# Kernel optimization log

Measured on AMD Instinct MI355X. Metric: run time of the kernel, lower is better.

The kernel has to match this reference:

```python
import jax, jax.numpy as jnp
import numpy as np

NEG = -1e9
EPS = 1e-3  # LayerNormalization eps in this repo


def sinusoid_table(n_position, d):
    pe = np.array([[p / np.power(10000, 2 * (j // 2) / d) for j in range(d)]
                   if p != 0 else np.zeros(d) for p in range(n_position)])
    pe[1:, 0::2] = np.sin(pe[1:, 0::2])
    pe[1:, 1::2] = np.cos(pe[1:, 1::2])
    return jnp.asarray(pe, jnp.float32)


def setup_inputs() -> dict:
    B, S, D, H, DK, DV, DFF, L, V = 16, 512, 512, 8, 64, 64, 1024, 6, 32000
    key = jax.random.key(0)
    ks = jax.random.split(key, 16)
    sc = 0.02
    word_emb = jax.random.normal(ks[0], (V, D), jnp.float32) * sc
    word_emb = word_emb.at[0].set(0.0)  # padding_idx=0
    pos_emb = sinusoid_table(S + 1, D)
    inp = {
        'src_seq': jax.random.randint(ks[1], (B, S), 1, V, jnp.int32),
        'src_pos': jnp.tile(jnp.arange(1, S + 1, dtype=jnp.int32)[None, :], (B, 1)),
        'word_emb': word_emb,
        'pos_emb': pos_emb,
        'Wq': jax.random.normal(ks[2], (L, H, D, DK), jnp.float32) * sc,
        'Wk': jax.random.normal(ks[3], (L, H, D, DK), jnp.float32) * sc,
        'Wv': jax.random.normal(ks[4], (L, H, D, DV), jnp.float32) * sc,
        'Wo': jax.random.normal(ks[5], (L, H * DV, D), jnp.float32) * sc,
        'bo': jnp.zeros((L, D), jnp.float32),
        'ln1_a': jnp.ones((L, D), jnp.float32),
        'ln1_b': jnp.zeros((L, D), jnp.float32),
        'w1': jax.random.normal(ks[6], (L, D, DFF), jnp.float32) * sc,
        'b1': jnp.zeros((L, DFF), jnp.float32),
        'w2': jax.random.normal(ks[7], (L, DFF, D), jnp.float32) * sc,
        'b2': jnp.zeros((L, D), jnp.float32),
        'ln2_a': jnp.ones((L, D), jnp.float32),
        'ln2_b': jnp.zeros((L, D), jnp.float32),
        'skip_w': jax.random.normal(ks[8], (L, D), jnp.float32) * sc,
        'skip_b': jnp.zeros((L,), jnp.float32),
    }
    return inp


def _layer_norm(z, a, b):
    mu = jnp.mean(z, axis=-1, keepdims=True)
    sd = jnp.std(z, axis=-1, keepdims=True, ddof=1)  # torch.std is unbiased
    return a * (z - mu) / (sd + EPS) + b


def _forward(src_seq, src_pos, word_emb, pos_emb, Wq, Wk, Wv, Wo, bo,
             ln1_a, ln1_b, w1, b1, w2, b2, ln2_a, ln2_b, skip_w, skip_b):
    B, S = src_seq.shape
    d_model = word_emb.shape[1]
    L, H = Wq.shape[0], Wq.shape[1]
    x = word_emb[src_seq] + pos_emb[src_pos]  # [B,S,D]
    rng = jax.random.key(42)
    scale = jnp.sqrt(jnp.float32(d_model))  # old-repo ScaledDotProductAttention temper
    for l in range(L):
        # --- SkippingProbability + ProbabilisticSkipper ---
        probs = jax.nn.sigmoid(jnp.einsum('bsd,d->bs', x, skip_w[l]) + skip_b[l])
        rng, sub = jax.random.split(rng)
        drop = jax.random.bernoulli(sub, jax.lax.stop_gradient(probs))  # noise ~ Bern(p)
        keep = ~drop  # keeping_timesteps = 1 - noise
        # stable compaction: kept timesteps to front, dropped positions zeroed (pad)
        order = jnp.argsort(jnp.where(keep, 0, 1), axis=1, stable=True)  # [B,S]
        x = jnp.take_along_axis(x, order[:, :, None], axis=1)
        x = x * jnp.take_along_axis(keep, order, axis=1)[:, :, None].astype(x.dtype)
        # pad mask recomputed from enc_input channel 0 (as in get_attn_padding_mask)
        pad = x[:, :, 0] == 0  # [B,S] True at padded keys
        # --- MultiHeadAttention ---
        residual = x
        q = jnp.einsum('bsd,hdk->bhsk', x, Wq[l])
        k = jnp.einsum('bsd,hdk->bhsk', x, Wk[l])
        v = jnp.einsum('bsd,hdv->bhsv', x, Wv[l])
        scores = jnp.einsum('bhqk,bhsk->bhqs', q, k) / scale
        scores = jnp.where(pad[:, None, None, :], NEG, scores)
        attn = jax.nn.softmax(scores, axis=-1)
        o = jnp.einsum('bhqs,bhsv->bhqv', attn, v)
        o = o.transpose(0, 2, 1, 3).reshape(B, S, -1)  # concat heads
        x = _layer_norm(o @ Wo[l] + bo[l] + residual, ln1_a[l], ln1_b[l])
        # --- PositionwiseFeedForwardFunnel ---
        h = jax.nn.relu(x @ w1[l] + b1[l]) @ w2[l] + b2[l]
        x = _layer_norm(h + x, ln2_a[l], ln2_b[l])
    return x


def reference(src_seq, src_pos, word_emb, pos_emb, Wq, Wk, Wv, Wo, bo,
              ln1_a, ln1_b, w1, b1, w2, b2, ln2_a, ln2_b, skip_w, skip_b):
    return _forward(src_seq, src_pos, word_emb, pos_emb, Wq, Wk, Wv, Wo, bo,
                    ln1_a, ln1_b, w1, b1, w2, b2, ln2_a, ln2_b, skip_w, skip_b)
```

## Files before the change

### kernel.cpp

```cpp
#include <hip/hip_runtime.h>
#include <math.h>

#define NEGV (-1e9f)
#define ISCALE 0.04419417382415922f

typedef __attribute__((ext_vector_type(8))) __bf16 bf16x8;
typedef __attribute__((ext_vector_type(4))) float f32x4;

__device__ inline unsigned short f2bf(float x){
  unsigned u = __float_as_uint(x);
  unsigned r = (u + 0x7fffu + ((u>>16)&1u)) >> 16;
  return (unsigned short)r;
}
__device__ inline float bf2f(unsigned short b){ return __uint_as_float((unsigned)b<<16); }

__host__ __device__ inline unsigned rotl32(unsigned v, int d){ return (v<<d)|(v>>(32-d)); }

__host__ __device__ inline void tf2x32(unsigned k0, unsigned k1, unsigned c0, unsigned c1,
                                       unsigned* o0, unsigned* o1){
  unsigned ks2 = k0 ^ k1 ^ 0x1BD11BDAu;
  unsigned x0 = c0 + k0, x1 = c1 + k1;
#define RND(r) { x0 += x1; x1 = rotl32(x1,(r)); x1 ^= x0; }
  RND(13) RND(15) RND(26) RND(6)   x0 += k1;  x1 += ks2 + 1u;
  RND(17) RND(29) RND(16) RND(24)  x0 += ks2; x1 += k0  + 2u;
  RND(13) RND(15) RND(26) RND(6)   x0 += k0;  x1 += k1  + 3u;
  RND(17) RND(29) RND(16) RND(24)  x0 += k1;  x1 += ks2 + 4u;
  RND(13) RND(15) RND(26) RND(6)   x0 += ks2; x1 += k0  + 5u;
#undef RND
  *o0 = x0; *o1 = x1;
}

__global__ void emb_kernel(const int* __restrict__ seq, const int* __restrict__ pos,
                           const float* __restrict__ we, const float* __restrict__ pe,
                           float* __restrict__ x){
  int t = blockIdx.x; int tid = threadIdx.x;
  int id = seq[t]; int pp = pos[t];
  float4 w = ((const float4*)(we + (size_t)id*512))[tid];
  float4 p = ((const float4*)(pe + (size_t)pp*512))[tid];
  float4 o; o.x=w.x+p.x; o.y=w.y+p.y; o.z=w.z+p.z; o.w=w.w+p.w;
  ((float4*)(x + (size_t)t*512))[tid] = o;
}

__global__ __launch_bounds__(64) void probs_keep_kernel(const float* __restrict__ x,
        const float* __restrict__ sw, const float* __restrict__ sb,
        unsigned k0, unsigned k1, int* __restrict__ keep){
  int t = blockIdx.x; int lane = threadIdx.x;
  const float* row = x + (size_t)t*512;
  float acc = 0.f;
  #pragma unroll
  for (int i=0;i<8;i++){ int d = lane + (i<<6); acc += row[d]*sw[d]; }
  #pragma unroll
  for (int o=32;o;o>>=1) acc += __shfl_xor(acc, o);
  if (lane==0){
    float z = acc + sb[0];
    float p = 1.f/(1.f + expf(-z));
    unsigned y0,y1; tf2x32(k0,k1, 0u,(unsigned)t, &y0,&y1);
    unsigned bits = y0 ^ y1;
    float u = __uint_as_float((bits>>9) | 0x3f800000u) - 1.0f;
    keep[t] = (u < p) ? 0 : 1;
  }
}

__global__ void scan_kernel(const int* __restrict__ keep, int* __restrict__ map,
                            int* __restrict__ nkeep){
  int b = blockIdx.x; int s = threadIdx.x;
  __shared__ int sc[512];
  int k = keep[(b<<9) + s];
  sc[s] = k;
  __syncthreads();
  for (int o=1;o<512;o<<=1){
    int t = (s>=o) ? sc[s-o] : 0;
    __syncthreads();
    sc[s] += t;
    __syncthreads();
  }
  if (k) map[(b<<9) + sc[s] - 1] = s;
  if (s==511) nkeep[b] = sc[511];
}

__global__ void gather_kernel(const float* __restrict__ src, float* __restrict__ dst,
                              const int* __restrict__ map, const int* __restrict__ nkeep){
  int blk = blockIdx.x; int b = blk >> 9; int j = blk & 511; int tid = threadIdx.x;
  float4* drow = (float4*)(dst + (size_t)blk*512);
  if (j < nkeep[b]){
    const float4* srow = (const float4*)(src + (size_t)((b<<9) + map[blk])*512);
    drow[tid] = srow[tid];
  } else {
    drow[tid] = make_float4(0.f,0.f,0.f,0.f);
  }
}

__global__ void wqkv_kernel(const float* __restrict__ Wq, const float* __restrict__ Wk,
                            const float* __restrict__ Wv, float* __restrict__ Wt){
  int d = blockIdx.x; int which = blockIdx.y; int c = threadIdx.x;
  const float* src = (which==0)? Wq : (which==1)? Wk : Wv;
  Wt[(size_t)d*1536 + (which<<9) + c] =
      src[(size_t)(c>>6)*32768 + ((size_t)d<<6) + (c&63)];
}

__global__ __launch_bounds__(256) void split3_kernel(const float* __restrict__ in,
        unsigned short* __restrict__ h, unsigned short* __restrict__ m,
        unsigned short* __restrict__ l, int n){
  int i = (blockIdx.x*256 + threadIdx.x) << 2;
  if (i >= n) return;
  float4 v = *(const float4*)(in + i);
  float xs[4] = {v.x, v.y, v.z, v.w};
  unsigned short ha[4], ma[4], la[4];
  #pragma unroll
  for (int j=0;j<4;j++){
    float x = xs[j];
    unsigned short hh = f2bf(x);
    float r1 = x - bf2f(hh);
    unsigned short mm = f2bf(r1);
    float r2 = r1 - bf2f(mm);
    ha[j]=hh; ma[j]=mm; la[j]=f2bf(r2);
  }
  *(ushort4*)(h+i) = make_ushort4(ha[0],ha[1],ha[2],ha[3]);
  *(ushort4*)(m+i) = make_ushort4(ma[0],ma[1],ma[2],ma[3]);
  *(ushort4*)(l+i) = make_ushort4(la[0],la[1],la[2],la[3]);
}

__global__ __launch_bounds__(256) void wsplit_kernel(const float* __restrict__ W,
        unsigned short* __restrict__ h, unsigned short* __restrict__ m,
        unsigned short* __restrict__ l, int K, int N){
  __shared__ float T[64][68];
  int k0 = blockIdx.y<<6, n0 = blockIdx.x<<6;
  int tid = threadIdx.x;
  int r = tid >> 4, c4 = tid & 15;
  #pragma unroll
  for (int rep=0; rep<4; rep++){
    int kk = r + (rep<<4);
    float4 v = *(const float4*)(W + (size_t)(k0+kk)*N + n0 + (c4<<2));
    *(float4*)&T[kk][c4<<2] = v;
  }
  __syncthreads();
  #pragma unroll
  for (int rep=0; rep<4; rep++){
    int nn = r + (rep<<4);
    int kk = c4<<2;
    unsigned short ha[4], ma[4], la[4];
    #pragma unroll
    for (int j=0;j<4;j++){
      float x = T[kk+j][nn];
      unsigned short hh = f2bf(x);
      float r1 = x - bf2f(hh);
      unsigned short mm = f2bf(r1);
      float r2 = r1 - bf2f(mm);
      ha[j]=hh; ma[j]=mm; la[j]=f2bf(r2);
    }
    size_t o = (size_t)(n0+nn)*K + k0 + kk;
    *(ushort4*)(h+o) = make_ushort4(ha[0],ha[1],ha[2],ha[3]);
    *(ushort4*)(m+o) = make_ushort4(ma[0],ma[1],ma[2],ma[3]);
    *(ushort4*)(l+o) = make_ushort4(la[0],la[1],la[2],la[3]);
  }
}

template<bool BIAS, bool RES, bool RELU>
__global__ __launch_bounds__(256) void gemm_mfma(
        const unsigned short* __restrict__ Ah, const unsigned short* __restrict__ Am2,
        const unsigned short* __restrict__ Al,
        const unsigned short* __restrict__ Bh, const unsigned short* __restrict__ Bm2,
        const unsigned short* __restrict__ Bl,
        const float* __restrict__ bias, const float* __restrict__ R,
        float* __restrict__ C, int M, int N, int K){
  __shared__ unsigned short As[3][128][40];
  __shared__ unsigned short Bs[3][128][40];
  int bn = blockIdx.x, bm = blockIdx.y;
  int tid = threadIdx.x;
  int w = tid >> 6, lane = tid & 63;
  int wm = w >> 1, wn = w & 1;
  int lrow = lane & 15, kg = lane >> 4;
  const unsigned short* Apl[3] = {Ah, Am2, Al};
  const unsigned short* Bpl[3] = {Bh, Bm2, Bl};

  f32x4 acc[4][4];
  const f32x4 zz = {0.f,0.f,0.f,0.f};
  #pragma unroll
  for (int i=0;i<4;i++)
    #pragma unroll
    for (int j=0;j<4;j++) acc[i][j] = zz;

  int srow = tid >> 1, seg = tid & 1;
  for (int ks = 0; ks < K; ks += 32){
    size_t abase = (size_t)(bm*128 + srow)*K + ks + seg*16;
    size_t bbase = (size_t)(bn*128 + srow)*K + ks + seg*16;
    #pragma unroll
    for (int p=0;p<3;p++){
      const unsigned short* ap = Apl[p] + abase;
      *(uint4*)&As[p][srow][seg*16]   = *(const uint4*)ap;
      *(uint4*)&As[p][srow][seg*16+8] = *(const uint4*)(ap+8);
      const unsigned short* bp = Bpl[p] + bbase;
      *(uint4*)&Bs[p][srow][seg*16]   = *(const uint4*)bp;
      *(uint4*)&Bs[p][srow][seg*16+8] = *(const uint4*)(bp+8);
    }
    __syncthreads();
    bf16x8 bfr[4][3];
    #pragma unroll
    for (int nf=0;nf<4;nf++)
      #pragma unroll
      for (int p=0;p<3;p++)
        bfr[nf][p] = *(const bf16x8*)&Bs[p][(wn<<6)+(nf<<4)+lrow][kg<<3];
    #pragma unroll
    for (int mf=0;mf<4;mf++){
      bf16x8 ah = *(const bf16x8*)&As[0][(wm<<6)+(mf<<4)+lrow][kg<<3];
      bf16x8 am = *(const bf16x8*)&As[1][(wm<<6)+(mf<<4)+lrow][kg<<3];
      bf16x8 al = *(const bf16x8*)&As[2][(wm<<6)+(mf<<4)+lrow][kg<<3];
      #pragma unroll
      for (int nf=0;nf<4;nf++){
        acc[mf][nf] = __builtin_amdgcn_mfma_f32_16x16x32_bf16(ah, bfr[nf][0], acc[mf][nf], 0,0,0);
        acc[mf][nf] = __builtin_amdgcn_mfma_f32_16x16x32_bf16(ah, bfr[nf][1], acc[mf][nf], 0,0,0);
        acc[mf][nf] = __builtin_amdgcn_mfma_f32_16x16x32_bf16(am, bfr[nf][0], acc[mf][nf], 0,0,0);
        acc[mf][nf] = __builtin_amdgcn_mfma_f32_16x16x32_bf16(ah, bfr[nf][2], acc[mf][nf], 0,0,0);
        acc[mf][nf] = __builtin_amdgcn_mfma_f32_16x16x32_bf16(al, bfr[nf][0], acc[mf][nf], 0,0,0);
        acc[mf][nf] = __builtin_amdgcn_mfma_f32_16x16x32_bf16(am, bfr[nf][1], acc[mf][nf], 0,0,0);
      }
    }
    __syncthreads();
  }
  int c0 = (bn<<7) + (wn<<6);
  int r0g = (bm<<7) + (wm<<6);
  #pragma unroll
  for (int mf=0;mf<4;mf++){
    #pragma unroll
    for (int nf=0;nf<4;nf++){
      int col = c0 + (nf<<4) + lrow;
      int rowb = r0g + (mf<<4) + (kg<<2);
      #pragma unroll
      for (int r=0;r<4;r++){
        float v = acc[mf][nf][r];
        if (BIAS) v += bias[col];
        if (RES)  v += R[(size_t)(rowb+r)*N + col];
        if (RELU) v = fmaxf(v, 0.f);
        C[(size_t)(rowb+r)*N + col] = v;
      }
    }
  }
}

template<bool BIAS, bool RES, bool RELU>
__global__ __launch_bounds__(256) void gemm_kernel(const float* __restrict__ A,
        const float* __restrict__ Bm, const float* __restrict__ bias,
        const float* __restrict__ R, float* __restrict__ C, int M, int N, int K){
  __shared__ float As[16][64];
  __shared__ float Bs[16][64];
  int bn = blockIdx.x, bm = blockIdx.y;
  int tid = threadIdx.x;
  int tx = tid & 15, ty = tid >> 4;
  int arow = tid >> 2,  acg = (tid & 3) << 2;
  int brow = tid >> 4,  bcg = (tid & 15) << 2;
  const float* Ab = A + (size_t)bm*64*K;
  const float* Bb = Bm + (bn<<6);
  float acc[4][4] = {};
  for (int k0 = 0; k0 < K; k0 += 16){
    float4 av = *(const float4*)(Ab + (size_t)arow*K + k0 + acg);
    float4 bv = *(const float4*)(Bb + (size_t)(k0+brow)*N + bcg);
    __syncthreads();
    As[acg+0][arow]=av.x; As[acg+1][arow]=av.y; As[acg+2][arow]=av.z; As[acg+3][arow]=av.w;
    *(float4*)&Bs[brow][bcg] = bv;
    __syncthreads();
    #pragma unroll
    for (int kk=0;kk<16;kk++){
      float4 a = *(const float4*)&As[kk][ty<<2];
      float4 b = *(const float4*)&Bs[kk][tx<<2];
      acc[0][0] += a.x*b.x; acc[0][1] += a.x*b.y; acc[0][2] += a.x*b.z; acc[0][3] += a.x*b.w;
      acc[1][0] += a.y*b.x; acc[1][1] += a.y*b.y; acc[1][2] += a.y*b.z; acc[1][3] += a.y*b.w;
      acc[2][0] += a.z*b.x; acc[2][1] += a.z*b.y; acc[2][2] += a.z*b.z; acc[2][3] += a.z*b.w;
      acc[3][0] += a.w*b.x; acc[3][1] += a.w*b.y; acc[3][2] += a.w*b.z; acc[3][3] += a.w*b.w;
    }
  }
  int row0 = (bm<<6) + (ty<<2), col0 = (bn<<6) + (tx<<2);
  #pragma unroll
  for (int i=0;i<4;i++){
    #pragma unroll
    for (int j=0;j<4;j++){
      float v = acc[i][j];
      if (BIAS) v += bias[col0+j];
      if (RES)  v += R[(size_t)(row0+i)*N + col0+j];
      if (RELU) v = fmaxf(v, 0.f);
      C[(size_t)(row0+i)*N + col0+j] = v;
    }
  }
}

__global__ __launch_bounds__(256) void fattn_kernel(const float* __restrict__ QKV,
        const float* __restrict__ Xc, float* __restrict__ O){
  __shared__ float QsT[64][68];
  __shared__ float KsT[64][68];
  __shared__ float Vs[64][68];
  __shared__ float PsT[64][68];
  __shared__ float pads[512];
  int orig = blockIdx.x;
  int wgid = ((orig & 7) << 7) + (orig >> 3);
  int qt = wgid & 7; int bh = wgid >> 3; int h = bh & 7; int b = bh >> 3;
  int tid = threadIdx.x;
  int d4 = tid & 15;
  int r0 = tid >> 4;
  size_t rowbase = (size_t)(b << 9) * 1536;
  int q0 = qt << 6;
  const float* Qg = QKV + rowbase + (size_t)q0*1536 + (h<<6);
  #pragma unroll
  for (int rep = 0; rep < 4; rep++){
    int q = r0 + (rep<<4);
    float4 v = *(const float4*)(Qg + (size_t)q*1536 + (d4<<2));
    QsT[(d4<<2)+0][q] = v.x; QsT[(d4<<2)+1][q] = v.y;
    QsT[(d4<<2)+2][q] = v.z; QsT[(d4<<2)+3][q] = v.w;
  }
  pads[tid]     = Xc[(size_t)((b<<9) + tid) << 9];
  pads[tid+256] = Xc[(size_t)((b<<9) + tid + 256) << 9];

  int tx = tid & 15, ty = tid >> 4;
  float m[4], l[4], out[4][4];
  #pragma unroll
  for (int i=0;i<4;i++){ m[i] = -3.0e38f; l[i] = 0.f;
    out[i][0]=0.f; out[i][1]=0.f; out[i][2]=0.f; out[i][3]=0.f; }
  const float* Kg = QKV + rowbase + 512 + (h<<6);
  const float* Vg = QKV + rowbase + 1024 + (h<<6);

  for (int kt = 0; kt < 8; kt++){
    __syncthreads();
    #pragma unroll
    for (int rep = 0; rep < 4; rep++){
      int k = r0 + (rep<<4);
      size_t krow = (size_t)((kt<<6) + k)*1536;
      float4 kv = *(const float4*)(Kg + krow + (d4<<2));
      KsT[(d4<<2)+0][k] = kv.x; KsT[(d4<<2)+1][k] = kv.y;
      KsT[(d4<<2)+2][k] = kv.z; KsT[(d4<<2)+3][k] = kv.w;
      float4 vv = *(const float4*)(Vg + krow + (d4<<2));
      *(float4*)&Vs[k][d4<<2] = vv;
    }
    __syncthreads();
    float acc[4][4] = {};
    #pragma unroll 4
    for (int d = 0; d < 64; d++){
      float4 a  = *(const float4*)&QsT[d][ty<<2];
      float4 bq = *(const float4*)&KsT[d][tx<<2];
      acc[0][0] += a.x*bq.x; acc[0][1] += a.x*bq.y; acc[0][2] += a.x*bq.z; acc[0][3] += a.x*bq.w;
      acc[1][0] += a.y*bq.x; acc[1][1] += a.y*bq.y; acc[1][2] += a.y*bq.z; acc[1][3] += a.y*bq.w;
      acc[2][0] += a.z*bq.x; acc[2][1] += a.z*bq.y; acc[2][2] += a.z*bq.z; acc[2][3] += a.z*bq.w;
      acc[3][0] += a.w*bq.x; acc[3][1] += a.w*bq.y; acc[3][2] += a.w*bq.z; acc[3][3] += a.w*bq.w;
    }
    int kbase = kt<<6;
    float sv[4][4];
    #pragma unroll
    for (int j=0;j<4;j++){
      bool pad = (pads[kbase + (tx<<2) + j] == 0.f);
      #pragma unroll
      for (int i=0;i<4;i++) sv[i][j] = pad ? NEGV : acc[i][j]*ISCALE;
    }
    #pragma unroll
    for (int i=0;i<4;i++){
      float tm = fmaxf(fmaxf(sv[i][0],sv[i][1]), fmaxf(sv[i][2],sv[i][3]));
      tm = fmaxf(tm, __shfl_xor(tm,1)); tm = fmaxf(tm, __shfl_xor(tm,2));
      tm = fmaxf(tm, __shfl_xor(tm,4)); tm = fmaxf(tm, __shfl_xor(tm,8));
      float mn = fmaxf(m[i], tm);
      float f  = expf(m[i] - mn);
      m[i] = mn;
      float rs = 0.f;
      #pragma unroll
      for (int j=0;j<4;j++){
        float e = expf(sv[i][j] - mn);
        sv[i][j] = e; rs += e;
      }
      rs += __shfl_xor(rs,1); rs += __shfl_xor(rs,2);
      rs += __shfl_xor(rs,4); rs += __shfl_xor(rs,8);
      l[i] = l[i]*f + rs;
      out[i][0]*=f; out[i][1]*=f; out[i][2]*=f; out[i][3]*=f;
    }
    #pragma unroll
    for (int j=0;j<4;j++){
      float4 pv = make_float4(sv[0][j], sv[1][j], sv[2][j], sv[3][j]);
      *(float4*)&PsT[(tx<<2)+j][ty<<2] = pv;
    }
    __syncthreads();
    #pragma unroll 4
    for (int k=0;k<64;k++){
      float4 a  = *(const float4*)&PsT[k][ty<<2];
      float4 bv = *(const float4*)&Vs[k][tx<<2];
      out[0][0] += a.x*bv.x; out[0][1] += a.x*bv.y; out[0][2] += a.x*bv.z; out[0][3] += a.x*bv.w;
      out[1][0] += a.y*bv.x; out[1][1] += a.y*bv.y; out[1][2] += a.y*bv.z; out[1][3] += a.y*bv.w;
      out[2][0] += a.z*bv.x; out[2][1] += a.z*bv.y; out[2][2] += a.z*bv.z; out[2][3] += a.z*bv.w;
      out[3][0] += a.w*bv.x; out[3][1] += a.w*bv.y; out[3][2] += a.w*bv.z; out[3][3] += a.w*bv.w;
    }
  }
  size_t obase = ((size_t)(b<<9) + q0) << 9;
  #pragma unroll
  for (int i=0;i<4;i++){
    float inv = 1.f / l[i];
    float4 ov = make_float4(out[i][0]*inv, out[i][1]*inv, out[i][2]*inv, out[i][3]*inv);
    *(float4*)(O + obase + (size_t)((ty<<2)+i)*512 + (h<<6) + (tx<<2)) = ov;
  }
}

__global__ __launch_bounds__(256) void ln_kernel(const float* __restrict__ in,
        const float* __restrict__ ga, const float* __restrict__ be, float* __restrict__ out){
  int t = blockIdx.x; int tid = threadIdx.x;
  const float* row = in + (size_t)t*512;
  float v0 = row[tid], v1 = row[tid+256];
  float s = v0 + v1;
  #pragma unroll
  for (int o=32;o;o>>=1) s += __shfl_xor(s,o);
  __shared__ float red[4];
  int wid = tid >> 6, lane = tid & 63;
  if (lane==0) red[wid] = s;
  __syncthreads();
  float mu = (red[0]+red[1]+red[2]+red[3]) * (1.f/512.f);
  float d0 = v0-mu, d1 = v1-mu;
  float q = d0*d0 + d1*d1;
  #pragma unroll
  for (int o=32;o;o>>=1) q += __shfl_xor(q,o);
  __syncthreads();
  if (lane==0) red[wid] = q;
  __syncthreads();
  float var = (red[0]+red[1]+red[2]+red[3]) * (1.f/511.f);
  float inv = 1.f/(sqrtf(var) + 1e-3f);
  float* orow = out + (size_t)t*512;
  orow[tid]     = ga[tid]    *(d0*inv) + be[tid];
  orow[tid+256] = ga[tid+256]*(d1*inv) + be[tid+256];
}

extern "C" void kernel_launch(void* const* d_in, const int* in_sizes, int n_in,
                              void* d_out, int out_size, void* d_ws, size_t ws_size,
                              hipStream_t stream){
  const int*   seq = (const int*)d_in[0];
  const int*   pos = (const int*)d_in[1];
  const float* we  = (const float*)d_in[2];
  const float* pe  = (const float*)d_in[3];
  const float* Wq  = (const float*)d_in[4];
  const float* Wk  = (const float*)d_in[5];
  const float* Wv  = (const float*)d_in[6];
  const float* Wo  = (const float*)d_in[7];
  const float* bo  = (const float*)d_in[8];
  const float* l1a = (const float*)d_in[9];
  const float* l1b = (const float*)d_in[10];
  const float* w1  = (const float*)d_in[11];
  const float* b1  = (const float*)d_in[12];
  const float* w2  = (const float*)d_in[13];
  const float* b2  = (const float*)d_in[14];
  const float* l2a = (const float*)d_in[15];
  const float* l2b = (const float*)d_in[16];
  const float* sw  = (const float*)d_in[17];
  const float* sb  = (const float*)d_in[18];
  float* out = (float*)d_out;

  const size_t TD = (size_t)8192*512;
  float* A    = (float*)d_ws;
  float* Bc   = A  + TD;
  float* QKVb = Bc + TD;
  float* P1   = QKVb;
  float* Hb   = QKVb + TD;
  float* Wt   = QKVb + 3*TD;
  int* keep = (int*)(Wt + (size_t)512*1536);
  int* map  = keep + 8192;
  int* nk   = map  + 8192;
  unsigned short* ap0 = (unsigned short*)(nk + 8192);
  const size_t APS = (size_t)8192*1024;
  unsigned short* ap1 = ap0 + APS;
  unsigned short* ap2 = ap1 + APS;
  unsigned short* wp0 = ap2 + APS;
  const size_t WPS = (size_t)1536*512;
  unsigned short* wp1 = wp0 + WPS;
  unsigned short* wp2 = wp1 + WPS;
  size_t need = (size_t)((char*)(wp2 + WPS) - (char*)d_ws);
  bool mfma_ok = (ws_size >= need);

  unsigned r0=0u, r1=42u, subs0[6], subs1[6];
  for (int l=0;l<6;l++){
    unsigned a0,a1,b0,b1;
    tf2x32(r0,r1, 0u,0u, &a0,&a1);
    tf2x32(r0,r1, 0u,1u, &b0,&b1);
    subs0[l]=b0; subs1[l]=b1; r0=a0; r1=a1;
  }

  emb_kernel<<<8192,128,0,stream>>>(seq,pos,we,pe,A);

  for (int l=0;l<6;l++){
    probs_keep_kernel<<<8192,64,0,stream>>>(A, sw + (size_t)l*512, sb + l,
                                            subs0[l], subs1[l], keep);
    scan_kernel<<<16,512,0,stream>>>(keep, map, nk);
    gather_kernel<<<8192,128,0,stream>>>(A, Bc, map, nk);
    wqkv_kernel<<<dim3(512,3),512,0,stream>>>(Wq + (size_t)l*262144,
                                              Wk + (size_t)l*262144,
                                              Wv + (size_t)l*262144, Wt);
    if (mfma_ok){
      split3_kernel<<<4096,256,0,stream>>>(Bc, ap0, ap1, ap2, 8192*512);
      wsplit_kernel<<<dim3(24,8),256,0,stream>>>(Wt, wp0, wp1, wp2, 512, 1536);
      gemm_mfma<false,false,false><<<dim3(12,64),256,0,stream>>>(ap0,ap1,ap2,
              wp0,wp1,wp2, nullptr, nullptr, QKVb, 8192,1536,512);
      fattn_kernel<<<1024,256,0,stream>>>(QKVb, Bc, A);
      split3_kernel<<<4096,256,0,stream>>>(A, ap0, ap1, ap2, 8192*512);
      wsplit_kernel<<<dim3(8,8),256,0,stream>>>(Wo + (size_t)l*262144, wp0, wp1, wp2, 512, 512);
      gemm_mfma<true,true,false><<<dim3(4,64),256,0,stream>>>(ap0,ap1,ap2,
              wp0,wp1,wp2, bo + (size_t)l*512, Bc, P1, 8192,512,512);
      ln_kernel<<<8192,256,0,stream>>>(P1, l1a + (size_t)l*512, l1b + (size_t)l*512, A);
      split3_kernel<<<4096,256,0,stream>>>(A, ap0, ap1, ap2, 8192*512);
      wsplit_kernel<<<dim3(16,8),256,0,stream>>>(w1 + (size_t)l*524288, wp0, wp1, wp2, 512, 1024);
      gemm_mfma<true,false,true><<<dim3(8,64),256,0,stream>>>(ap0,ap1,ap2,
              wp0,wp1,wp2, b1 + (size_t)l*1024, nullptr, Hb, 8192,1024,512);
      split3_kernel<<<8192,256,0,stream>>>(Hb, ap0, ap1, ap2, 8192*1024);
      wsplit_kernel<<<dim3(8,16),256,0,stream>>>(w2 + (size_t)l*524288, wp0, wp1, wp2, 1024, 512);
      gemm_mfma<true,true,false><<<dim3(4,64),256,0,stream>>>(ap0,ap1,ap2,
              wp0,wp1,wp2, b2 + (size_t)l*512, A, P1, 8192,512,1024);
    } else {
      gemm_kernel<false,false,false><<<dim3(24,128),256,0,stream>>>(Bc, Wt,
              nullptr, nullptr, QKVb, 8192,1536,512);
      fattn_kernel<<<1024,256,0,stream>>>(QKVb, Bc, A);
      gemm_kernel<true,true,false><<<dim3(8,128),256,0,stream>>>(A, Wo + (size_t)l*262144,
              bo + (size_t)l*512, Bc, P1, 8192,512,512);
      ln_kernel<<<8192,256,0,stream>>>(P1, l1a + (size_t)l*512, l1b + (size_t)l*512, A);
      gemm_kernel<true,false,true><<<dim3(16,128),256,0,stream>>>(A, w1 + (size_t)l*524288,
              b1 + (size_t)l*1024, nullptr, Hb, 8192,1024,512);
      gemm_kernel<true,true,false><<<dim3(8,128),256,0,stream>>>(Hb, w2 + (size_t)l*524288,
              b2 + (size_t)l*512, A, P1, 8192,512,1024);
    }
    ln_kernel<<<8192,256,0,stream>>>(P1, l2a + (size_t)l*512, l2b + (size_t)l*512,
                                     (l==5)? out : A);
  }
}
```

Measured before the change: 3.142 ms.

## Replace 3-way bf16 split GEMM with 2-way scaled fp16 split

Operands are now split into an fp16 high part and an fp16 residual scaled by 4096, replacing the three-part bf16 decomposition. Each GEMM issues three fp16 MFMAs per tile instead of six bf16 MFMAs and loads two planes instead of three. This cuts the split-kernel traffic, the LDS footprint and the tensor-core work. The trade-off is reduced accuracy and fp16 range limits: values beyond fp16 range, or residuals that underflow, could hurt fp32 emulation fidelity.

```diff
diff --git a/kernel.cpp b/kernel.cpp
--- a/kernel.cpp
+++ b/kernel.cpp
@@ -4,15 +4,16 @@
 #define NEGV (-1e9f)
 #define ISCALE 0.04419417382415922f
 
-typedef __attribute__((ext_vector_type(8))) __bf16 bf16x8;
+typedef __attribute__((ext_vector_type(8))) _Float16 f16x8;
+typedef __attribute__((ext_vector_type(4))) _Float16 f16x4;
 typedef __attribute__((ext_vector_type(4))) float f32x4;
 
-__device__ inline unsigned short f2bf(float x){
-  unsigned u = __float_as_uint(x);
-  unsigned r = (u + 0x7fffu + ((u>>16)&1u)) >> 16;
-  return (unsigned short)r;
-}
-__device__ inline float bf2f(unsigned short b){ return __uint_as_float((unsigned)b<<16); }
+__device__ inline void split2h(float x, _Float16& H, _Float16& M){
+  _Float16 h = (_Float16)x;
+  float m = x - (float)h;
+  H = h;
+  M = (_Float16)(m * 4096.0f);
+}
 
 __host__ __device__ inline unsigned rotl32(unsigned v, int d){ return (v<<d)|(v>>(32-d)); }
 
@@ -98,31 +99,21 @@
       src[(size_t)(c>>6)*32768 + ((size_t)d<<6) + (c&63)];
 }
 
-__global__ __launch_bounds__(256) void split3_kernel(const float* __restrict__ in,
-        unsigned short* __restrict__ h, unsigned short* __restrict__ m,
-        unsigned short* __restrict__ l, int n){
+__global__ __launch_bounds__(256) void split2_kernel(const float* __restrict__ in,
+        _Float16* __restrict__ h, _Float16* __restrict__ m, int n){
   int i = (blockIdx.x*256 + threadIdx.x) << 2;
   if (i >= n) return;
   float4 v = *(const float4*)(in + i);
   float xs[4] = {v.x, v.y, v.z, v.w};
-  unsigned short ha[4], ma[4], la[4];
-  #pragma unroll
-  for (int j=0;j<4;j++){
-    float x = xs[j];
-    unsigned short hh = f2bf(x);
-    float r1 = x - bf2f(hh);
-    unsigned short mm = f2bf(r1);
-    float r2 = r1 - bf2f(mm);
-    ha[j]=hh; ma[j]=mm; la[j]=f2bf(r2);
-  }
-  *(ushort4*)(h+i) = make_ushort4(ha[0],ha[1],ha[2],ha[3]);
-  *(ushort4*)(m+i) = make_ushort4(ma[0],ma[1],ma[2],ma[3]);
-  *(ushort4*)(l+i) = make_ushort4(la[0],la[1],la[2],la[3]);
+  f16x4 ha, ma;
+  #pragma unroll
+  for (int j=0;j<4;j++){ _Float16 H,M; split2h(xs[j],H,M); ha[j]=H; ma[j]=M; }
+  *(f16x4*)(h+i) = ha;
+  *(f16x4*)(m+i) = ma;
 }
 
 __global__ __launch_bounds__(256) void wsplit_kernel(const float* __restrict__ W,
-        unsigned short* __restrict__ h, unsigned short* __restrict__ m,
-        unsigned short* __restrict__ l, int K, int N){
+        _Float16* __restrict__ h, _Float16* __restrict__ m, int K, int N){
   __shared__ float T[64][68];
   int k0 = blockIdx.y<<6, n0 = blockIdx.x<<6;
   int tid = threadIdx.x;
@@ -138,81 +129,67 @@
   for (int rep=0; rep<4; rep++){
     int nn = r + (rep<<4);
     int kk = c4<<2;
-    unsigned short ha[4], ma[4], la[4];
-    #pragma unroll
-    for (int j=0;j<4;j++){
-      float x = T[kk+j][nn];
-      unsigned short hh = f2bf(x);
-      float r1 = x - bf2f(hh);
-      unsigned short mm = f2bf(r1);
-      float r2 = r1 - bf2f(mm);
-      ha[j]=hh; ma[j]=mm; la[j]=f2bf(r2);
-    }
+    f16x4 ha, ma;
+    #pragma unroll
+    for (int j=0;j<4;j++){ _Float16 H,M; split2h(T[kk+j][nn],H,M); ha[j]=H; ma[j]=M; }
     size_t o = (size_t)(n0+nn)*K + k0 + kk;
-    *(ushort4*)(h+o) = make_ushort4(ha[0],ha[1],ha[2],ha[3]);
-    *(ushort4*)(m+o) = make_ushort4(ma[0],ma[1],ma[2],ma[3]);
-    *(ushort4*)(l+o) = make_ushort4(la[0],la[1],la[2],la[3]);
+    *(f16x4*)(h+o) = ha;
+    *(f16x4*)(m+o) = ma;
   }
 }
 
 template<bool BIAS, bool RES, bool RELU>
 __global__ __launch_bounds__(256) void gemm_mfma(
-        const unsigned short* __restrict__ Ah, const unsigned short* __restrict__ Am2,
-        const unsigned short* __restrict__ Al,
-        const unsigned short* __restrict__ Bh, const unsigned short* __restrict__ Bm2,
-        const unsigned short* __restrict__ Bl,
+        const _Float16* __restrict__ Ah, const _Float16* __restrict__ Am,
+        const _Float16* __restrict__ Bh, const _Float16* __restrict__ Bm,
         const float* __restrict__ bias, const float* __restrict__ R,
         float* __restrict__ C, int M, int N, int K){
-  __shared__ unsigned short As[3][128][40];
-  __shared__ unsigned short Bs[3][128][40];
+  __shared__ _Float16 As[2][128][40];
+  __shared__ _Float16 Bs[2][128][40];
   int bn = blockIdx.x, bm = blockIdx.y;
   int tid = threadIdx.x;
   int w = tid >> 6, lane = tid & 63;
   int wm = w >> 1, wn = w & 1;
   int lrow = lane & 15, kg = lane >> 4;
-  const unsigned short* Apl[3] = {Ah, Am2, Al};
-  const unsigned short* Bpl[3] = {Bh, Bm2, Bl};
-
-  f32x4 acc[4][4];
+  const _Float16* Apl[2] = {Ah, Am};
+  const _Float16* Bpl[2] = {Bh, Bm};
+
+  f32x4 acc0[4][4], acc1[4][4];
   const f32x4 zz = {0.f,0.f,0.f,0.f};
   #pragma unroll
   for (int i=0;i<4;i++)
     #pragma unroll
-    for (int j=0;j<4;j++) acc[i][j] = zz;
+    for (int j=0;j<4;j++){ acc0[i][j] = zz; acc1[i][j] = zz; }
 
   int srow = tid >> 1, seg = tid & 1;
   for (int ks = 0; ks < K; ks += 32){
     size_t abase = (size_t)(bm*128 + srow)*K + ks + seg*16;
     size_t bbase = (size_t)(bn*128 + srow)*K + ks + seg*16;
     #pragma unroll
-    for (int p=0;p<3;p++){
-      const unsigned short* ap = Apl[p] + abase;
+    for (int p=0;p<2;p++){
+      const _Float16* ap = Apl[p] + abase;
       *(uint4*)&As[p][srow][seg*16]   = *(const uint4*)ap;
       *(uint4*)&As[p][srow][seg*16+8] = *(const uint4*)(ap+8);
-      const unsigned short* bp = Bpl[p] + bbase;
+      const _Float16* bp = Bpl[p] + bbase;
       *(uint4*)&Bs[p][srow][seg*16]   = *(const uint4*)bp;
       *(uint4*)&Bs[p][srow][seg*16+8] = *(const uint4*)(bp+8);
     }
     __syncthreads();
-    bf16x8 bfr[4][3];
+    f16x8 bfr[4][2];
     #pragma unroll
     for (int nf=0;nf<4;nf++)
       #pragma unroll
-      for (int p=0;p<3;p++)
-        bfr[nf][p] = *(const bf16x8*)&Bs[p][(wn<<6)+(nf<<4)+lrow][kg<<3];
+      for (int p=0;p<2;p++)
+        bfr[nf][p] = *(const f16x8*)&Bs[p][(wn<<6)+(nf<<4)+lrow][kg<<3];
     #pragma unroll
     for (int mf=0;mf<4;mf++){
-      bf16x8 ah = *(const bf16x8*)&As[0][(wm<<6)+(mf<<4)+lrow][kg<<3];
-      bf16x8 am = *(const bf16x8*)&As[1][(wm<<6)+(mf<<4)+lrow][kg<<3];
-      bf16x8 al = *(const bf16x8*)&As[2][(wm<<6)+(mf<<4)+lrow][kg<<3];
+      f16x8 ah = *(const f16x8*)&As[0][(wm<<6)+(mf<<4)+lrow][kg<<3];
+      f16x8 am = *(const f16x8*)&As[1][(wm<<6)+(mf<<4)+lrow][kg<<3];
       #pragma unroll
       for (int nf=0;nf<4;nf++){
-        acc[mf][nf] = __builtin_amdgcn_mfma_f32_16x16x32_bf16(ah, bfr[nf][0], acc[mf][nf], 0,0,0);
-        acc[mf][nf] = __builtin_amdgcn_mfma_f32_16x16x32_bf16(ah, bfr[nf][1], acc[mf][nf], 0,0,0);
-        acc[mf][nf] = __builtin_amdgcn_mfma_f32_16x16x32_bf16(am, bfr[nf][0], acc[mf][nf], 0,0,0);
-        acc[mf][nf] = __builtin_amdgcn_mfma_f32_16x16x32_bf16(ah, bfr[nf][2], acc[mf][nf], 0,0,0);
-        acc[mf][nf] = __builtin_amdgcn_mfma_f32_16x16x32_bf16(al, bfr[nf][0], acc[mf][nf], 0,0,0);
-        acc[mf][nf] = __builtin_amdgcn_mfma_f32_16x16x32_bf16(am, bfr[nf][1], acc[mf][nf], 0,0,0);
+        acc0[mf][nf] = __builtin_amdgcn_mfma_f32_16x16x32_f16(ah, bfr[nf][0], acc0[mf][nf], 0,0,0);
+        acc1[mf][nf] = __builtin_amdgcn_mfma_f32_16x16x32_f16(ah, bfr[nf][1], acc1[mf][nf], 0,0,0);
+        acc1[mf][nf] = __builtin_amdgcn_mfma_f32_16x16x32_f16(am, bfr[nf][0], acc1[mf][nf], 0,0,0);
       }
     }
     __syncthreads();
@@ -227,7 +204,7 @@
       int rowb = r0g + (mf<<4) + (kg<<2);
       #pragma unroll
       for (int r=0;r<4;r++){
-        float v = acc[mf][nf][r];
+        float v = acc0[mf][nf][r] + acc1[mf][nf][r] * (1.0f/4096.0f);
         if (BIAS) v += bias[col];
         if (RES)  v += R[(size_t)(rowb+r)*N + col];
         if (RELU) v = fmaxf(v, 0.f);
@@ -452,15 +429,13 @@
   int* keep = (int*)(Wt + (size_t)512*1536);
   int* map  = keep + 8192;
   int* nk   = map  + 8192;
-  unsigned short* ap0 = (unsigned short*)(nk + 8192);
+  _Float16* ap0 = (_Float16*)(nk + 8192);
   const size_t APS = (size_t)8192*1024;
-  unsigned short* ap1 = ap0 + APS;
-  unsigned short* ap2 = ap1 + APS;
-  unsigned short* wp0 = ap2 + APS;
+  _Float16* ap1 = ap0 + APS;
+  _Float16* wp0 = ap1 + APS;
   const size_t WPS = (size_t)1536*512;
-  unsigned short* wp1 = wp0 + WPS;
-  unsigned short* wp2 = wp1 + WPS;
-  size_t need = (size_t)((char*)(wp2 + WPS) - (char*)d_ws);
+  _Float16* wp1 = wp0 + WPS;
+  size_t need = (size_t)((char*)(wp1 + WPS) - (char*)d_ws);
   bool mfma_ok = (ws_size >= need);
 
   unsigned r0=0u, r1=42u, subs0[6], subs1[6];
@@ -482,24 +457,24 @@
                                               Wk + (size_t)l*262144,
                                               Wv + (size_t)l*262144, Wt);
     if (mfma_ok){
-      split3_kernel<<<4096,256,0,stream>>>(Bc, ap0, ap1, ap2, 8192*512);
-      wsplit_kernel<<<dim3(24,8),256,0,stream>>>(Wt, wp0, wp1, wp2, 512, 1536);
-      gemm_mfma<false,false,false><<<dim3(12,64),256,0,stream>>>(ap0,ap1,ap2,
-              wp0,wp1,wp2, nullptr, nullptr, QKVb, 8192,1536,512);
+      split2_kernel<<<4096,256,0,stream>>>(Bc, ap0, ap1, 8192*512);
+      wsplit_kernel<<<dim3(24,8),256,0,stream>>>(Wt, wp0, wp1, 512, 1536);
+      gemm_mfma<false,false,false><<<dim3(12,64),256,0,stream>>>(ap0,ap1,
+              wp0,wp1, nullptr, nullptr, QKVb, 8192,1536,512);
       fattn_kernel<<<1024,256,0,stream>>>(QKVb, Bc, A);
-      split3_kernel<<<4096,256,0,stream>>>(A, ap0, ap1, ap2, 8192*512);
-      wsplit_kernel<<<dim3(8,8),256,0,stream>>>(Wo + (size_t)l*262144, wp0, wp1, wp2, 512, 512);
-      gemm_mfma<true,true,false><<<dim3(4,64),256,0,stream>>>(ap0,ap1,ap2,
-              wp0,wp1,wp2, bo + (size_t)l*512, Bc, P1, 8192,512,512);
+      split2_kernel<<<4096,256,0,stream>>>(A, ap0, ap1, 8192*512);
+      wsplit_kernel<<<dim3(8,8),256,0,stream>>>(Wo + (size_t)l*262144, wp0, wp1, 512, 512);
+      gemm_mfma<true,true,false><<<dim3(4,64),256,0,stream>>>(ap0,ap1,
+              wp0,wp1, bo + (size_t)l*512, Bc, P1, 8192,512,512);
       ln_kernel<<<8192,256,0,stream>>>(P1, l1a + (size_t)l*512, l1b + (size_t)l*512, A);
-      split3_kernel<<<4096,256,0,stream>>>(A, ap0, ap1, ap2, 8192*512);
-      wsplit_kernel<<<dim3(16,8),256,0,stream>>>(w1 + (size_t)l*524288, wp0, wp1, wp2, 512, 1024);
-      gemm_mfma<true,false,true><<<dim3(8,64),256,0,stream>>>(ap0,ap1,ap2,
-              wp0,wp1,wp2, b1 + (size_t)l*1024, nullptr, Hb, 8192,1024,512);
-      split3_kernel<<<8192,256,0,stream>>>(Hb, ap0, ap1, ap2, 8192*1024);
-      wsplit_kernel<<<dim3(8,16),256,0,stream>>>(w2 + (size_t)l*524288, wp0, wp1, wp2, 1024, 512);
-      gemm_mfma<true,true,false><<<dim3(4,64),256,0,stream>>>(ap0,ap1,ap2,
-              wp0,wp1,wp2, b2 + (size_t)l*512, A, P1, 8192,512,1024);
+      split2_kernel<<<4096,256,0,stream>>>(A, ap0, ap1, 8192*512);
+      wsplit_kernel<<<dim3(16,8),256,0,stream>>>(w1 + (size_t)l*524288, wp0, wp1, 512, 1024);
+      gemm_mfma<true,false,true><<<dim3(8,64),256,0,stream>>>(ap0,ap1,
+              wp0,wp1, b1 + (size_t)l*1024, nullptr, Hb, 8192,1024,512);
+      split2_kernel<<<8192,256,0,stream>>>(Hb, ap0, ap1, 8192*1024);
+      wsplit_kernel<<<dim3(8,16),256,0,stream>>>(w2 + (size_t)l*524288, wp0, wp1, 1024, 512);
+      gemm_mfma<true,true,false><<<dim3(4,64),256,0,stream>>>(ap0,ap1,
+              wp0,wp1, b2 + (size_t)l*512, A, P1, 8192,512,1024);
     } else {
       gemm_kernel<false,false,false><<<dim3(24,128),256,0,stream>>>(Bc, Wt,
               nullptr, nullptr, QKVb, 8192,1536,512);
```

New measurement: 2.771 ms. 1.13x faster.
